# Optimization experiments

Measured on AMD Instinct MI355X. Metric: run time of the kernel, lower is better.

The kernel has to match this reference:

```python
import jax, jax.numpy as jnp
import numpy as np


def setup_inputs() -> dict:
    key = jax.random.key(0)
    k1, k2, k3 = jax.random.split(key, 3)
    N, M, D, C = 4096, 8192, 1024, 128
    x = jax.random.normal(k1, (N, D), dtype=jnp.float32)
    x_n = jax.random.normal(k2, (M, D), dtype=jnp.float32)
    y = jax.random.uniform(k3, (M, C), dtype=jnp.float32)
    # module parameter: log_T = log(init_temperature) = log(1.0) = 0.0
    log_T = jnp.array(0.0, dtype=jnp.float32)
    return {"x": x, "x_n": x_n, "y": y, "log_T": log_T}


def reference(x, x_n, y, log_T):
    # Faithful to NONA.forward with similarity='euclidean', batch_norm=None,
    # agg=None, and x != x_n (plain softmax branch, no diagonal mask).
    T = jnp.exp(log_T)  # computed in the original forward but never applied
    del T
    # sim = -cdist(x, x_n, p=2)  via the ||a-b||^2 = ||a||^2 + ||b||^2 - 2ab expansion
    x_sq = jnp.sum(x * x, axis=1, keepdims=True)          # [N, 1]
    xn_sq = jnp.sum(x_n * x_n, axis=1)                    # [M]
    d2 = x_sq + xn_sq[None, :] - 2.0 * (x @ x_n.T)        # [N, M]
    sim = -jnp.sqrt(jnp.maximum(d2, 0.0))                 # [N, M]
    sim_scores = jax.nn.softmax(sim, axis=1)              # [N, M]
    return sim_scores @ y                                 # [N, C]
```

## Files before the change

### kernel.cpp

```cpp
#include <hip/hip_runtime.h>


#define N_ 4096
#define M_ 8192
#define D_ 1024
#define C_ 128
#define SPLIT 16
#define MCOLS (M_ / SPLIT)
#define NBN (MCOLS / 128)
#define NKK (D_ / 64)

typedef __bf16 bf16;
typedef __attribute__((ext_vector_type(8))) __bf16 bf16x8;
typedef __attribute__((ext_vector_type(4))) __bf16 bf16x4;
typedef __attribute__((ext_vector_type(4))) float f32x4;

__device__ __forceinline__ void async_copy16(const bf16* gp, void* lp) {
  __builtin_amdgcn_global_load_lds(
      (__attribute__((address_space(1))) void*)const_cast<bf16*>(gp),
      (__attribute__((address_space(3))) void*)lp, 16, 0, 0);
}

__device__ __forceinline__ int swz(int row, int gran) {
  return (row << 7) + ((gran ^ (row & 7)) << 4);
}
__device__ __forceinline__ int swz2(int row, int gran) {
  return (row << 8) + ((gran ^ (row & 15)) << 4);
}

__device__ __forceinline__ void stage16(const bf16* src, char* lds, int tid) {
  const int lane = tid & 63, wave = tid >> 6;
#pragma unroll
  for (int j = 0; j < 4; ++j) {
    const int ch  = j * 4 + wave;
    const int off = ch * 1024 + lane * 16;
    const int row = off >> 7;
    const int gr  = ((off >> 4) & 7) ^ (row & 7);
    async_copy16(src + (size_t)row * D_ + gr * 8, lds + ch * 1024);
  }
}
__device__ __forceinline__ void stageV(const bf16* yT, int colbase, char* lds, int tid) {
  const int lane = tid & 63, wave = tid >> 6;
#pragma unroll
  for (int j = 0; j < 8; ++j) {
    const int ch  = j * 4 + wave;
    const int off = ch * 1024 + lane * 16;
    const int row = off >> 8;
    const int gr  = ((off >> 4) & 15) ^ (row & 15);
    async_copy16(yT + (size_t)row * M_ + colbase + gr * 8, lds + ch * 1024);
  }
}

#define VM0 asm volatile("s_waitcnt vmcnt(0)" ::: "memory")

__global__ __launch_bounds__(256, 2)
void nona_main(const bf16* __restrict__ xb, const bf16* __restrict__ xnb,
               const bf16* __restrict__ yT, const float* __restrict__ xsq,
               const float* __restrict__ xnsq, float* __restrict__ Opart,
               float* __restrict__ Lpart)
{
  __shared__ __align__(16) char Lds[65536];
  char* const A0 = Lds;
  char* const A1 = Lds + 16384;
  char* const B0 = Lds + 32768;
  char* const B1 = Lds + 49152;
  char* const Pb = A0;
  char* const Vb = B0;

  const int tid  = threadIdx.x;
  const int lane = tid & 63;
  const int wave = tid >> 6;
  const int wr = wave >> 1, wc = wave & 1;
  const int g = lane >> 4, c = lane & 15;

  const int xcd = blockIdx.x & 7;
  const int idx = blockIdx.x >> 3;
  const int rb  = ((xcd >> 2) << 4) | (idx >> 2);
  const int s   = ((xcd & 3) << 2) | (idx & 3);
  const int row0 = rb * 128;
  const int col0 = s * MCOLS;

  const bf16* xA = xb + (size_t)row0 * D_;

  float xs[4];
#pragma unroll
  for (int rf = 0; rf < 4; ++rf)
    xs[rf] = xsq[row0 + wr * 64 + rf * 16 + c];

  f32x4 Oacc[4][4];
  const f32x4 zero = {0.f, 0.f, 0.f, 0.f};
#pragma unroll
  for (int rf = 0; rf < 4; ++rf)
#pragma unroll
    for (int cc = 0; cc < 4; ++cc) Oacc[rf][cc] = zero;
  float lsum[4] = {0.f, 0.f, 0.f, 0.f};

#pragma unroll 1
  for (int bn = 0; bn < NBN; ++bn) {
    const int colbase = col0 + bn * 128;
    const bf16* xB = xnb + (size_t)colbase * D_;

    f32x4 Sacc[4][4];
#pragma unroll
    for (int rf = 0; rf < 4; ++rf)
#pragma unroll
      for (int cf = 0; cf < 4; ++cf) Sacc[rf][cf] = zero;

    stage16(xA, A0, tid);
    stage16(xB, B0, tid);

#pragma unroll 1
    for (int kk = 0; kk < NKK; ++kk) {
      VM0;
      __builtin_amdgcn_s_barrier();
      __builtin_amdgcn_sched_barrier(0);
      const char* Ac = (kk & 1) ? A1 : A0;
      const char* Bc = (kk & 1) ? B1 : B0;
      {
        bf16x8 af[4], bv[4];
#pragma unroll
        for (int rf = 0; rf < 4; ++rf)
          af[rf] = *(const bf16x8*)(Ac + swz(wr * 64 + rf * 16 + c, g));
#pragma unroll
        for (int j = 0; j < 4; ++j)
          bv[j] = *(const bf16x8*)(Bc + swz(wc * 64 + j * 16 + c, g));
        if (kk < NKK - 1) {
          stage16(xA + (kk + 1) * 64, (kk & 1) ? A0 : A1, tid);
          stage16(xB + (kk + 1) * 64, (kk & 1) ? B0 : B1, tid);
        }
        __builtin_amdgcn_s_setprio(1);
#pragma unroll
        for (int j = 0; j < 4; ++j)
#pragma unroll
          for (int rf = 0; rf < 4; ++rf)
            Sacc[rf][j] = __builtin_amdgcn_mfma_f32_16x16x32_bf16(
                bv[j], af[rf], Sacc[rf][j], 0, 0, 0);
        __builtin_amdgcn_s_setprio(0);
      }
      {
        bf16x8 af[4], bv[4];
#pragma unroll
        for (int rf = 0; rf < 4; ++rf)
          af[rf] = *(const bf16x8*)(Ac + swz(wr * 64 + rf * 16 + c, 4 + g));
#pragma unroll
        for (int j = 0; j < 4; ++j)
          bv[j] = *(const bf16x8*)(Bc + swz(wc * 64 + j * 16 + c, 4 + g));
        __builtin_amdgcn_s_setprio(1);
#pragma unroll
        for (int j = 0; j < 4; ++j)
#pragma unroll
          for (int rf = 0; rf < 4; ++rf)
            Sacc[rf][j] = __builtin_amdgcn_mfma_f32_16x16x32_bf16(
                bv[j], af[rf], Sacc[rf][j], 0, 0, 0);
        __builtin_amdgcn_s_setprio(0);
      }
    }
    __syncthreads();

    stageV(yT, colbase, Vb, tid);

#pragma unroll
    for (int cf = 0; cf < 4; ++cf) {
      const float4 nsq4 = *(const float4*)(xnsq + colbase + wc * 64 + cf * 16 + g * 4);
#pragma unroll
      for (int rf = 0; rf < 4; ++rf)
#pragma unroll
        for (int r = 0; r < 4; ++r) {
          float d2 = xs[rf] + ((const float*)&nsq4)[r] - 2.0f * Sacc[rf][cf][r];
          d2 = fmaxf(d2, 0.0f);
          const float wv = __expf(-sqrtf(d2));
          lsum[rf] += wv;
          Sacc[rf][cf][r] = wv;
        }
    }

#pragma unroll
    for (int rf = 0; rf < 4; ++rf)
#pragma unroll
      for (int cf = 0; cf < 4; ++cf) {
        bf16x4 pk;
#pragma unroll
        for (int r = 0; r < 4; ++r) pk[r] = (bf16)Sacc[rf][cf][r];
        const int prow = wr * 64 + rf * 16 + c;
        const int gran = wc * 8 + cf * 2 + (g >> 1);
        *(bf16x4*)(Pb + (prow << 8) + ((gran ^ (prow & 15)) << 4) + (g & 1) * 8) = pk;
      }
    __syncthreads();

#pragma unroll
    for (int ks = 0; ks < 4; ++ks) {
      bf16x8 pa[4], vb[4];
#pragma unroll
      for (int rf = 0; rf < 4; ++rf)
        pa[rf] = *(const bf16x8*)(Pb + swz2(wr * 64 + rf * 16 + c, ks * 4 + g));
#pragma unroll
      for (int cc = 0; cc < 4; ++cc)
        vb[cc] = *(const bf16x8*)(Vb + swz2(wc * 64 + cc * 16 + c, ks * 4 + g));
      __builtin_amdgcn_s_setprio(1);
#pragma unroll
      for (int cc = 0; cc < 4; ++cc)
#pragma unroll
        for (int rf = 0; rf < 4; ++rf)
          Oacc[rf][cc] = __builtin_amdgcn_mfma_f32_16x16x32_bf16(pa[rf], vb[cc], Oacc[rf][cc], 0, 0, 0);
      __builtin_amdgcn_s_setprio(0);
    }
    __syncthreads();
  }

  float* Lr = (float*)Lds;
#pragma unroll
  for (int rf = 0; rf < 4; ++rf) {
    float v = lsum[rf];
    v += __shfl_xor(v, 16);
    v += __shfl_xor(v, 32);
    if (g == 0) Lr[wc * 128 + wr * 64 + rf * 16 + c] = v;
  }
  __syncthreads();
  if (tid < 128)
    Lpart[(size_t)s * N_ + row0 + tid] = Lr[tid] + Lr[128 + tid];

  float* ob = Opart + ((size_t)s * N_ + row0) * C_;
#pragma unroll
  for (int rf = 0; rf < 4; ++rf)
#pragma unroll
    for (int cc = 0; cc < 4; ++cc)
#pragma unroll
      for (int r = 0; r < 4; ++r)
        ob[(wr * 64 + rf * 16 + g * 4 + r) * C_ + wc * 64 + cc * 16 + c] = Oacc[rf][cc][r];
}

__global__ void prep_all(const float* __restrict__ x, const float* __restrict__ xn,
                         const float* __restrict__ y,
                         bf16* __restrict__ xb, bf16* __restrict__ xnb,
                         bf16* __restrict__ yT,
                         float* __restrict__ xsq, float* __restrict__ xnsq)
{
  const int blk = blockIdx.x;
  const int t = threadIdx.x;
  if (blk < N_ + M_) {
    const float* src; bf16* dst; float* sq; int row;
    if (blk < N_) { src = x;  dst = xb;  sq = xsq;  row = blk; }
    else          { src = xn; dst = xnb; sq = xnsq; row = blk - N_; }
    const float4 v = reinterpret_cast<const float4*>(src + (size_t)row * D_)[t];
    float ss = v.x * v.x + v.y * v.y + v.z * v.z + v.w * v.w;
    bf16x4 hv;
    hv[0] = (bf16)v.x; hv[1] = (bf16)v.y; hv[2] = (bf16)v.z; hv[3] = (bf16)v.w;
    *reinterpret_cast<bf16x4*>(dst + (size_t)row * D_ + t * 4) = hv;
#pragma unroll
    for (int o = 32; o > 0; o >>= 1) ss += __shfl_down(ss, o);
    __shared__ float red[4];
    if ((t & 63) == 0) red[t >> 6] = ss;
    __syncthreads();
    if (t == 0) sq[row] = red[0] + red[1] + red[2] + red[3];
  } else {
    __shared__ bf16 tile[C_][72];
    const int m0 = (blk - (N_ + M_)) * 64;
#pragma unroll
    for (int i = 0; i < 32; ++i) {
      const int idx = i * 256 + t;
      const int ml = idx >> 7, cc = idx & 127;
      tile[cc][ml] = (bf16)y[(size_t)(m0 + ml) * C_ + cc];
    }
    __syncthreads();
#pragma unroll
    for (int i = 0; i < 32; ++i) {
      const int idx = i * 256 + t;
      const int cc = idx >> 6, ml = idx & 63;
      yT[(size_t)cc * M_ + m0 + ml] = tile[cc][ml];
    }
  }
}

__global__ void combine(const float* __restrict__ Opart, const float* __restrict__ Lpart,
                        float* __restrict__ out)
{
  const int i = blockIdx.x * 256 + threadIdx.x;
  const int row = i >> 7;
  float o = 0.f, l = 0.f;
#pragma unroll
  for (int s = 0; s < SPLIT; ++s) {
    o += Opart[(size_t)s * N_ * C_ + i];
    l += Lpart[(size_t)s * N_ + row];
  }
  out[i] = o / l;
}

extern "C" void kernel_launch(void* const* d_in, const int* in_sizes, int n_in,
                              void* d_out, int out_size, void* d_ws, size_t ws_size,
                              hipStream_t stream)
{
  const float* x  = (const float*)d_in[0];
  const float* xn = (const float*)d_in[1];
  const float* y  = (const float*)d_in[2];
  float* out = (float*)d_out;

  char* ws = (char*)d_ws;
  bf16*  xb    = (bf16*)(ws);
  bf16*  xnb   = (bf16*)(ws + (size_t)8  * 1024 * 1024);
  bf16*  yT    = (bf16*)(ws + (size_t)24 * 1024 * 1024);
  float* xsq   = (float*)(ws + (size_t)26 * 1024 * 1024);
  float* xnsq  = (float*)(ws + (size_t)26 * 1024 * 1024 + 16 * 1024);
  float* Lpart = (float*)(ws + (size_t)26 * 1024 * 1024 + 64 * 1024);
  float* Opart = (float*)(ws + (size_t)27 * 1024 * 1024);

  prep_all<<<N_ + M_ + M_ / 64, 256, 0, stream>>>(x, xn, y, xb, xnb, yT, xsq, xnsq);
  nona_main<<<32 * SPLIT, 256, 0, stream>>>(xb, xnb, yT, xsq, xnsq, Opart, Lpart);
  combine<<<(N_ * C_) / 256, 256, 0, stream>>>(Opart, Lpart, out);
}
```

Before: 121.9 us.

## Cut LDS footprint to fit three blocks per CU and double the M split

The x tile is now single-buffered in LDS, with an extra barrier before its next k-slice is loaded, and y^T is staged in two 64-column halves. Together these shrink shared memory from 64 KB to 48 KB, and launch bounds are raised to three blocks per CU. The M dimension is split 32 ways instead of 16, so there are twice as many blocks with half the columns each, and the block-index mapping is changed to match. This aims to raise occupancy and hide latency. In exchange it adds barriers, removes the prefetch overlap for the A tile, and increases the partial-sum reduction work and the wave-quantization tail.

```diff
diff --git a/kernel.cpp b/kernel.cpp
--- a/kernel.cpp
+++ b/kernel.cpp
@@ -5,7 +5,7 @@
 #define M_ 8192
 #define D_ 1024
 #define C_ 128
-#define SPLIT 16
+#define SPLIT 32
 #define MCOLS (M_ / SPLIT)
 #define NBN (MCOLS / 128)
 #define NKK (D_ / 64)
@@ -28,7 +28,7 @@
   return (row << 8) + ((gran ^ (row & 15)) << 4);
 }
 
-__device__ __forceinline__ void stage16(const bf16* src, char* lds, int tid) {
+__device__ __forceinline__ void stage16(const bf16* src, int ld, char* lds, int tid) {
   const int lane = tid & 63, wave = tid >> 6;
 #pragma unroll
   for (int j = 0; j < 4; ++j) {
@@ -36,36 +36,25 @@
     const int off = ch * 1024 + lane * 16;
     const int row = off >> 7;
     const int gr  = ((off >> 4) & 7) ^ (row & 7);
-    async_copy16(src + (size_t)row * D_ + gr * 8, lds + ch * 1024);
-  }
-}
-__device__ __forceinline__ void stageV(const bf16* yT, int colbase, char* lds, int tid) {
-  const int lane = tid & 63, wave = tid >> 6;
-#pragma unroll
-  for (int j = 0; j < 8; ++j) {
-    const int ch  = j * 4 + wave;
-    const int off = ch * 1024 + lane * 16;
-    const int row = off >> 8;
-    const int gr  = ((off >> 4) & 15) ^ (row & 15);
-    async_copy16(yT + (size_t)row * M_ + colbase + gr * 8, lds + ch * 1024);
+    async_copy16(src + (size_t)row * ld + gr * 8, lds + ch * 1024);
   }
 }
 
 #define VM0 asm volatile("s_waitcnt vmcnt(0)" ::: "memory")
-
-__global__ __launch_bounds__(256, 2)
+#define LGKM0 asm volatile("s_waitcnt lgkmcnt(0)" ::: "memory")
+
+__global__ __launch_bounds__(256, 3)
 void nona_main(const bf16* __restrict__ xb, const bf16* __restrict__ xnb,
                const bf16* __restrict__ yT, const float* __restrict__ xsq,
                const float* __restrict__ xnsq, float* __restrict__ Opart,
                float* __restrict__ Lpart)
 {
-  __shared__ __align__(16) char Lds[65536];
-  char* const A0 = Lds;
-  char* const A1 = Lds + 16384;
-  char* const B0 = Lds + 32768;
-  char* const B1 = Lds + 49152;
-  char* const Pb = A0;
-  char* const Vb = B0;
+  __shared__ __align__(16) char Lds[49152];
+  char* const Am = Lds;
+  char* const B0 = Lds + 16384;
+  char* const B1 = Lds + 32768;
+  char* const Pb = Lds;
+  char* const Vb = B1;
 
   const int tid  = threadIdx.x;
   const int lane = tid & 63;
@@ -75,8 +64,8 @@
 
   const int xcd = blockIdx.x & 7;
   const int idx = blockIdx.x >> 3;
-  const int rb  = ((xcd >> 2) << 4) | (idx >> 2);
-  const int s   = ((xcd & 3) << 2) | (idx & 3);
+  const int rb  = ((xcd >> 2) << 4) | (idx >> 3);
+  const int s   = ((xcd & 3) << 3) | (idx & 7);
   const int row0 = rb * 128;
   const int col0 = s * MCOLS;
 
@@ -106,28 +95,26 @@
 #pragma unroll
       for (int cf = 0; cf < 4; ++cf) Sacc[rf][cf] = zero;
 
-    stage16(xA, A0, tid);
-    stage16(xB, B0, tid);
+    stage16(xA, D_, Am, tid);
+    stage16(xB, D_, B0, tid);
 
 #pragma unroll 1
     for (int kk = 0; kk < NKK; ++kk) {
       VM0;
       __builtin_amdgcn_s_barrier();
       __builtin_amdgcn_sched_barrier(0);
-      const char* Ac = (kk & 1) ? A1 : A0;
       const char* Bc = (kk & 1) ? B1 : B0;
+      char* const Bn = (kk & 1) ? B0 : B1;
       {
         bf16x8 af[4], bv[4];
 #pragma unroll
         for (int rf = 0; rf < 4; ++rf)
-          af[rf] = *(const bf16x8*)(Ac + swz(wr * 64 + rf * 16 + c, g));
+          af[rf] = *(const bf16x8*)(Am + swz(wr * 64 + rf * 16 + c, g));
 #pragma unroll
         for (int j = 0; j < 4; ++j)
           bv[j] = *(const bf16x8*)(Bc + swz(wc * 64 + j * 16 + c, g));
-        if (kk < NKK - 1) {
-          stage16(xA + (kk + 1) * 64, (kk & 1) ? A0 : A1, tid);
-          stage16(xB + (kk + 1) * 64, (kk & 1) ? B0 : B1, tid);
-        }
+        if (kk < NKK - 1)
+          stage16(xB + (kk + 1) * 64, D_, Bn, tid);
         __builtin_amdgcn_s_setprio(1);
 #pragma unroll
         for (int j = 0; j < 4; ++j)
@@ -141,10 +128,15 @@
         bf16x8 af[4], bv[4];
 #pragma unroll
         for (int rf = 0; rf < 4; ++rf)
-          af[rf] = *(const bf16x8*)(Ac + swz(wr * 64 + rf * 16 + c, 4 + g));
+          af[rf] = *(const bf16x8*)(Am + swz(wr * 64 + rf * 16 + c, 4 + g));
 #pragma unroll
         for (int j = 0; j < 4; ++j)
           bv[j] = *(const bf16x8*)(Bc + swz(wc * 64 + j * 16 + c, 4 + g));
+        LGKM0;
+        __builtin_amdgcn_sched_barrier(0);
+        __builtin_amdgcn_s_barrier();
+        if (kk < NKK - 1)
+          stage16(xA + (kk + 1) * 64, D_, Am, tid);
         __builtin_amdgcn_s_setprio(1);
 #pragma unroll
         for (int j = 0; j < 4; ++j)
@@ -157,7 +149,7 @@
     }
     __syncthreads();
 
-    stageV(yT, colbase, Vb, tid);
+    stage16(yT + colbase, M_, Vb, tid);
 
 #pragma unroll
     for (int cf = 0; cf < 4; ++cf) {
@@ -188,14 +180,35 @@
     __syncthreads();
 
 #pragma unroll
-    for (int ks = 0; ks < 4; ++ks) {
+    for (int ks = 0; ks < 2; ++ks) {
       bf16x8 pa[4], vb[4];
 #pragma unroll
       for (int rf = 0; rf < 4; ++rf)
         pa[rf] = *(const bf16x8*)(Pb + swz2(wr * 64 + rf * 16 + c, ks * 4 + g));
 #pragma unroll
       for (int cc = 0; cc < 4; ++cc)
-        vb[cc] = *(const bf16x8*)(Vb + swz2(wc * 64 + cc * 16 + c, ks * 4 + g));
+        vb[cc] = *(const bf16x8*)(Vb + swz(wc * 64 + cc * 16 + c, ks * 4 + g));
+      __builtin_amdgcn_s_setprio(1);
+#pragma unroll
+      for (int cc = 0; cc < 4; ++cc)
+#pragma unroll
+        for (int rf = 0; rf < 4; ++rf)
+          Oacc[rf][cc] = __builtin_amdgcn_mfma_f32_16x16x32_bf16(pa[rf], vb[cc], Oacc[rf][cc], 0, 0, 0);
+      __builtin_amdgcn_s_setprio(0);
+    }
+    __syncthreads();
+    stage16(yT + colbase + 64, M_, Vb, tid);
+    __syncthreads();
+
+#pragma unroll
+    for (int ks = 0; ks < 2; ++ks) {
+      bf16x8 pa[4], vb[4];
+#pragma unroll
+      for (int rf = 0; rf < 4; ++rf)
+        pa[rf] = *(const bf16x8*)(Pb + swz2(wr * 64 + rf * 16 + c, (2 + ks) * 4 + g));
+#pragma unroll
+      for (int cc = 0; cc < 4; ++cc)
+        vb[cc] = *(const bf16x8*)(Vb + swz(wc * 64 + cc * 16 + c, ks * 4 + g));
       __builtin_amdgcn_s_setprio(1);
 #pragma unroll
       for (int cc = 0; cc < 4; ++cc)
```

Result: slower. 177.7 us (+45.7%).

## Fuse split-K combine into main kernel via last-block atomic counter

Applied to the files above, without the earlier changes.

Removes the separate combine kernel launch. Each main-kernel block now bumps a per-row-block atomic counter after writing its partials, and the last of the SPLIT blocks for a row block sums the partial outputs and normalisers and writes the final result. The counters are zeroed inside the prep kernel. This saves one launch and its tail, but the reduction now runs on only 32 blocks and adds fences and an atomic at every block's end.

```diff
diff --git a/kernel.cpp b/kernel.cpp
--- a/kernel.cpp
+++ b/kernel.cpp
@@ -57,7 +57,8 @@
 void nona_main(const bf16* __restrict__ xb, const bf16* __restrict__ xnb,
                const bf16* __restrict__ yT, const float* __restrict__ xsq,
                const float* __restrict__ xnsq, float* __restrict__ Opart,
-               float* __restrict__ Lpart)
+               float* __restrict__ Lpart, int* __restrict__ cnt,
+               float* __restrict__ out)
 {
   __shared__ __align__(16) char Lds[65536];
   char* const A0 = Lds;
@@ -227,16 +228,51 @@
 #pragma unroll
       for (int r = 0; r < 4; ++r)
         ob[(wr * 64 + rf * 16 + g * 4 + r) * C_ + wc * 64 + cc * 16 + c] = Oacc[rf][cc][r];
+
+  __threadfence();
+  __syncthreads();
+  int* flag = (int*)Lds;
+  if (tid == 0)
+    flag[0] = (int)__hip_atomic_fetch_add(&cnt[rb], 1, __ATOMIC_ACQ_REL,
+                                          __HIP_MEMORY_SCOPE_AGENT);
+  __syncthreads();
+  if (flag[0] != SPLIT - 1) return;
+  __threadfence();
+
+  float* lsh = (float*)(Lds + 64);
+  if (tid < 128) {
+    float l = 0.f;
+#pragma unroll
+    for (int ss = 0; ss < SPLIT; ++ss)
+      l += Lpart[(size_t)ss * N_ + row0 + tid];
+    lsh[tid] = 1.0f / l;
+  }
+  __syncthreads();
+
+  const size_t base = (size_t)row0 * C_;
+  for (int i = tid * 4; i < 128 * C_; i += 256 * 4) {
+    float4 o = {0.f, 0.f, 0.f, 0.f};
+#pragma unroll
+    for (int ss = 0; ss < SPLIT; ++ss) {
+      const float4 p = *(const float4*)(Opart + (size_t)ss * N_ * C_ + base + i);
+      o.x += p.x; o.y += p.y; o.z += p.z; o.w += p.w;
+    }
+    const float li = lsh[i >> 7];
+    float4 r; r.x = o.x * li; r.y = o.y * li; r.z = o.z * li; r.w = o.w * li;
+    *(float4*)(out + base + i) = r;
+  }
 }
 
 __global__ void prep_all(const float* __restrict__ x, const float* __restrict__ xn,
                          const float* __restrict__ y,
                          bf16* __restrict__ xb, bf16* __restrict__ xnb,
                          bf16* __restrict__ yT,
-                         float* __restrict__ xsq, float* __restrict__ xnsq)
+                         float* __restrict__ xsq, float* __restrict__ xnsq,
+                         int* __restrict__ cnt)
 {
   const int blk = blockIdx.x;
   const int t = threadIdx.x;
+  if (blk == 0 && t < 32) cnt[t] = 0;
   if (blk < N_ + M_) {
     const float* src; bf16* dst; float* sq; int row;
     if (blk < N_) { src = x;  dst = xb;  sq = xsq;  row = blk; }
@@ -271,20 +307,6 @@
   }
 }
 
-__global__ void combine(const float* __restrict__ Opart, const float* __restrict__ Lpart,
-                        float* __restrict__ out)
-{
-  const int i = blockIdx.x * 256 + threadIdx.x;
-  const int row = i >> 7;
-  float o = 0.f, l = 0.f;
-#pragma unroll
-  for (int s = 0; s < SPLIT; ++s) {
-    o += Opart[(size_t)s * N_ * C_ + i];
-    l += Lpart[(size_t)s * N_ + row];
-  }
-  out[i] = o / l;
-}
-
 extern "C" void kernel_launch(void* const* d_in, const int* in_sizes, int n_in,
                               void* d_out, int out_size, void* d_ws, size_t ws_size,
                               hipStream_t stream)
@@ -301,9 +323,11 @@
   float* xsq   = (float*)(ws + (size_t)26 * 1024 * 1024);
   float* xnsq  = (float*)(ws + (size_t)26 * 1024 * 1024 + 16 * 1024);
   float* Lpart = (float*)(ws + (size_t)26 * 1024 * 1024 + 64 * 1024);
+  int*   cnt   = (int*)  (ws + (size_t)26 * 1024 * 1024 + 512 * 1024);
   float* Opart = (float*)(ws + (size_t)27 * 1024 * 1024);
 
-  prep_all<<<N_ + M_ + M_ / 64, 256, 0, stream>>>(x, xn, y, xb, xnb, yT, xsq, xnsq);
-  nona_main<<<32 * SPLIT, 256, 0, stream>>>(xb, xnb, yT, xsq, xnsq, Opart, Lpart);
-  combine<<<(N_ * C_) / 256, 256, 0, stream>>>(Opart, Lpart, out);
-}
+  prep_all<<<N_ + M_ + M_ / 64, 256, 0, stream>>>(x, xn, y, xb, xnb, yT,
+                                                  xsq, xnsq, cnt);
+  nona_main<<<32 * SPLIT, 256, 0, stream>>>(xb, xnb, yT, xsq, xnsq,
+                                            Opart, Lpart, cnt, out);
+}
```

Measured after the change: 226.9 us. 1.86x slower.
